# Optimization experiments

Measured on AMD Instinct MI355X. Metric: run time of the kernel, lower is better.

## Reference

```python
import jax, jax.numpy as jnp
from jax import lax
import numpy as np

E = 16          # n_routed_experts
H = 2048        # hidden_size
I = 1408        # moe_intermediate_size
T = 2048        # tokens
K = 6           # top_k


def setup_inputs() -> dict:
    key = jax.random.key(0)
    k1, k2, k3, k4, k5 = jax.random.split(key, 5)
    hidden_states = jax.random.normal(k1, (T, H), dtype=jnp.float32)
    top_k_index = jax.random.randint(k2, (T, K), 0, E)
    top_k_weights = jax.random.uniform(k3, (T, K), dtype=jnp.float32)
    gate_up_proj = jax.random.normal(k4, (E, 2 * I, H), dtype=jnp.float32) * 0.02
    down_proj = jax.random.normal(k5, (E, H, I), dtype=jnp.float32) * 0.02
    return {
        "hidden_states": hidden_states,
        "top_k_index": top_k_index,
        "top_k_weights": top_k_weights,
        "gate_up_proj": gate_up_proj,
        "down_proj": down_proj,
    }


def reference(hidden_states, top_k_index, top_k_weights, gate_up_proj, down_proj):
    # combine[t, e] = sum over k-slots of top_k_weights[t, k] where top_k_index[t, k] == e
    # (scatter-add handles duplicate expert picks identically to index_add_).
    n_tok = hidden_states.shape[0]
    n_exp = gate_up_proj.shape[0]
    combine = jnp.zeros((n_tok, n_exp), hidden_states.dtype)
    combine = combine.at[jnp.arange(n_tok)[:, None], top_k_index].add(top_k_weights)

    def expert_step(acc, params):
        gu, dn, c_e = params  # gu: [2I, H], dn: [H, I], c_e: [n_tok]
        gate, up = jnp.split(hidden_states @ gu.T, 2, axis=-1)  # each [n_tok, I]
        y = (jax.nn.silu(gate) * up) @ dn.T                     # [n_tok, H]
        return acc + y * c_e[:, None], None

    out, _ = lax.scan(
        expert_step,
        jnp.zeros_like(hidden_states),
        (gate_up_proj, down_proj, combine.T),
    )
    return out
```

## Files before the change

kernel.cpp:

```cpp
#include <hip/hip_runtime.h>
#include <hip/hip_bf16.h>
#include <cstdint>

#define T_TOK 2048
#define HD 2048
#define ID 1408
#define NE 16
#define TOPK 6

#define BM 256
#define BK 64
#define BN 32
#define NT1 44
#define NT2 64
#define GMAX 64

typedef __bf16 bf16x8 __attribute__((ext_vector_type(8)));
typedef float f32x4 __attribute__((ext_vector_type(4)));

typedef const __attribute__((address_space(1))) void* gas1_t;
typedef __attribute__((address_space(3))) void* las3_t;
#define GLDS16(g, l) __builtin_amdgcn_global_load_lds((gas1_t)(g), (las3_t)(l), 16, 0, 0)


__global__ void k_combine(const int* __restrict__ idx, const float* __restrict__ w,
                          float* __restrict__ combine) {
    int t = blockIdx.x * blockDim.x + threadIdx.x;
    if (t >= T_TOK) return;
    int ie[TOPK];
    float fw[TOPK];
#pragma unroll
    for (int k = 0; k < TOPK; k++) { ie[k] = idx[t * TOPK + k]; fw[k] = w[t * TOPK + k]; }
#pragma unroll
    for (int e = 0; e < NE; e++) {
        float s = 0.f;
#pragma unroll
        for (int k = 0; k < TOPK; k++) if (ie[k] == e) s += fw[k];
        combine[t * NE + e] = s;
    }
}

__global__ void k_lists(const float* __restrict__ combine, int* __restrict__ counts,
                        int* __restrict__ tok, float* __restrict__ wts) {
    int t = blockIdx.x * blockDim.x + threadIdx.x;
    if (t >= T_TOK) return;
    for (int e = 0; e < NE; e++) {
        float c = combine[t * NE + e];
        if (c != 0.0f) {
            int p = atomicAdd(&counts[e], 1);
            tok[e * T_TOK + p] = t;
            wts[e * T_TOK + p] = c;
        }
    }
}

__global__ void k_cvt(const float* __restrict__ x, __bf16* __restrict__ xb) {
    int i = (blockIdx.x * 256 + threadIdx.x) * 8;
    float4 a = *(const float4*)(x + i);
    float4 b = *(const float4*)(x + i + 4);
    bf16x8 o;
    o[0] = (__bf16)a.x; o[1] = (__bf16)a.y; o[2] = (__bf16)a.z; o[3] = (__bf16)a.w;
    o[4] = (__bf16)b.x; o[5] = (__bf16)b.y; o[6] = (__bf16)b.z; o[7] = (__bf16)b.w;
    *(bf16x8*)(xb + i) = o;
}

__global__ void k_cvtw(const float* __restrict__ src, __bf16* __restrict__ dst, int n8) {
    int stride = gridDim.x * blockDim.x;
    for (int i = blockIdx.x * blockDim.x + threadIdx.x; i < n8; i += stride) {
        size_t o = (size_t)i * 8;
        float4 a = *(const float4*)(src + o);
        float4 b = *(const float4*)(src + o + 4);
        bf16x8 v;
        v[0] = (__bf16)a.x; v[1] = (__bf16)a.y; v[2] = (__bf16)a.z; v[3] = (__bf16)a.w;
        v[4] = (__bf16)b.x; v[5] = (__bf16)b.y; v[6] = (__bf16)b.z; v[7] = (__bf16)b.w;
        *(bf16x8*)(dst + o) = v;
    }
}


__device__ __forceinline__ int swz(int row, int cb) {
    return row * 128 + (cb ^ ((row & 7) << 4));
}

__device__ __forceinline__ bf16x8 ldfrag(const __bf16* base, int row, int cb) {
    return *(const bf16x8*)((const char*)base + swz(row, cb));
}

__device__ __forceinline__ void stage8(const float* __restrict__ src, char* lds,
                                       int row, int cb) {
    float4 f0 = ((const float4*)src)[0];
    float4 f1 = ((const float4*)src)[1];
    bf16x8 o;
    o[0] = (__bf16)f0.x; o[1] = (__bf16)f0.y; o[2] = (__bf16)f0.z; o[3] = (__bf16)f0.w;
    o[4] = (__bf16)f1.x; o[5] = (__bf16)f1.y; o[6] = (__bf16)f1.z; o[7] = (__bf16)f1.w;
    *(bf16x8*)(lds + swz(row, cb)) = o;
}

__device__ __forceinline__ bool decode_item(const int* __restrict__ counts, int it,
                                            int ntn, int& e, int& m, int& n, int& cnt) {
    int r = it;
    for (int ee = 0; ee < NE; ee++) {
        int c = counts[ee];
        int nm = (c + BM - 1) >> 8;
        int tot = nm * ntn;
        if (r < tot) { e = ee; m = r % nm; n = r / nm; cnt = c; return true; }
        r -= tot;
    }
    return false;
}


__global__ __launch_bounds__(256, 4) void k_gemm1_bf16(
    const __bf16* __restrict__ Xb, const __bf16* __restrict__ wgu,
    const int* __restrict__ counts, const int* __restrict__ tok,
    __bf16* __restrict__ act) {
    __shared__ __align__(16) __bf16 sA[BM * BK];
    __shared__ __align__(16) __bf16 sBg[BN * BK];
    __shared__ __align__(16) __bf16 sBu[BN * BK];

    int e, m, n, cnt;
    if (!decode_item(counts, blockIdx.x, NT1, e, m, n, cnt)) return;
    int m0 = m * BM;
    int n0 = n * BN;

    int tid = threadIdx.x;
    int lane = tid & 63;
    int wid = tid >> 6;
    int l15 = lane & 15, lh = lane >> 4;
    int csw = ((lane & 7) ^ ((lane >> 3) & 7)) * 8;

    const __bf16* pA[8];
#pragma unroll
    for (int j = 0; j < 8; j++) {
        int r = 64 * wid + 8 * j + (lane >> 3);
        int g = m0 + r;
        if (g >= cnt) g = cnt - 1;
        pA[j] = Xb + (size_t)tok[e * T_TOK + g] * HD + csw;
    }

    int brow = 8 * wid + (lane >> 3);
    int bsw = ((lane & 7) ^ (lane >> 3)) * 8;
    const __bf16* wbase = wgu + (size_t)e * (2 * ID) * HD;
    const __bf16* pBg = wbase + (size_t)(n0 + brow) * HD + bsw;
    const __bf16* pBu = wbase + (size_t)(ID + n0 + brow) * HD + bsw;

    f32x4 accg[4][2] = {};
    f32x4 accu[4][2] = {};

    for (int k0 = 0; k0 < HD; k0 += BK) {
        __syncthreads();
#pragma unroll
        for (int j = 0; j < 8; j++)
            GLDS16(pA[j] + k0, &sA[(64 * wid + 8 * j) * BK]);
        GLDS16(pBg + k0, &sBg[wid * 512]);
        GLDS16(pBu + k0, &sBu[wid * 512]);
        __syncthreads();
#pragma unroll
        for (int kk = 0; kk < 2; kk++) {
            int cb = kk * 64 + lh * 16;
            bf16x8 a[4];
#pragma unroll
            for (int fm = 0; fm < 4; fm++)
                a[fm] = ldfrag(sA, wid * 64 + fm * 16 + l15, cb);
#pragma unroll
            for (int fn = 0; fn < 2; fn++) {
                bf16x8 bg = ldfrag(sBg, fn * 16 + l15, cb);
                bf16x8 bu = ldfrag(sBu, fn * 16 + l15, cb);
#pragma unroll
                for (int fm = 0; fm < 4; fm++) {
                    accg[fm][fn] = __builtin_amdgcn_mfma_f32_16x16x32_bf16(a[fm], bg, accg[fm][fn], 0, 0, 0);
                    accu[fm][fn] = __builtin_amdgcn_mfma_f32_16x16x32_bf16(a[fm], bu, accu[fm][fn], 0, 0, 0);
                }
            }
        }
    }

#pragma unroll
    for (int fm = 0; fm < 4; fm++) {
#pragma unroll
        for (int fn = 0; fn < 2; fn++) {
#pragma unroll
            for (int j = 0; j < 4; j++) {
                int mloc = wid * 64 + fm * 16 + lh * 4 + j;
                int g = m0 + mloc;
                if (g < cnt) {
                    float gv = accg[fm][fn][j];
                    float uv = accu[fm][fn][j];
                    float sv = gv * (1.0f / (1.0f + __expf(-gv)));
                    int nn = n0 + fn * 16 + l15;
                    act[((size_t)e * T_TOK + g) * ID + nn] = (__bf16)(sv * uv);
                }
            }
        }
    }
}


__global__ __launch_bounds__(256, 4) void k_gemm1_f32(
    const __bf16* __restrict__ Xb, const float* __restrict__ gup,
    const int* __restrict__ counts, const int* __restrict__ tok,
    __bf16* __restrict__ act) {
    __shared__ __align__(16) __bf16 sA[BM * BK];
    __shared__ __align__(16) __bf16 sBg[BN * BK];
    __shared__ __align__(16) __bf16 sBu[BN * BK];

    int e, m, n, cnt;
    if (!decode_item(counts, blockIdx.x, NT1, e, m, n, cnt)) return;
    int m0 = m * BM;
    int n0 = n * BN;

    int tid = threadIdx.x;
    int lane = tid & 63;
    int wid = tid >> 6;
    int l15 = lane & 15, lh = lane >> 4;
    int csw = ((lane & 7) ^ ((lane >> 3) & 7)) * 8;

    const __bf16* pA[8];
#pragma unroll
    for (int j = 0; j < 8; j++) {
        int r = 64 * wid + 8 * j + (lane >> 3);
        int g = m0 + r;
        if (g >= cnt) g = cnt - 1;
        pA[j] = Xb + (size_t)tok[e * T_TOK + g] * HD + csw;
    }

    int br = tid >> 3, bc = tid & 7;
    const float* gbase = gup + (size_t)e * (2 * ID) * HD;
    const float* bgSrc = gbase + (size_t)(n0 + br) * HD + bc * 8;
    const float* buSrc = gbase + (size_t)(ID + n0 + br) * HD + bc * 8;

    f32x4 accg[4][2] = {};
    f32x4 accu[4][2] = {};

    for (int k0 = 0; k0 < HD; k0 += BK) {
        __syncthreads();
#pragma unroll
        for (int j = 0; j < 8; j++)
            GLDS16(pA[j] + k0, &sA[(64 * wid + 8 * j) * BK]);
        stage8(bgSrc + k0, (char*)sBg, br, bc * 16);
        stage8(buSrc + k0, (char*)sBu, br, bc * 16);
        __syncthreads();
#pragma unroll
        for (int kk = 0; kk < 2; kk++) {
            int cb = kk * 64 + lh * 16;
            bf16x8 a[4];
#pragma unroll
            for (int fm = 0; fm < 4; fm++)
                a[fm] = ldfrag(sA, wid * 64 + fm * 16 + l15, cb);
#pragma unroll
            for (int fn = 0; fn < 2; fn++) {
                bf16x8 bg = ldfrag(sBg, fn * 16 + l15, cb);
                bf16x8 bu = ldfrag(sBu, fn * 16 + l15, cb);
#pragma unroll
                for (int fm = 0; fm < 4; fm++) {
                    accg[fm][fn] = __builtin_amdgcn_mfma_f32_16x16x32_bf16(a[fm], bg, accg[fm][fn], 0, 0, 0);
                    accu[fm][fn] = __builtin_amdgcn_mfma_f32_16x16x32_bf16(a[fm], bu, accu[fm][fn], 0, 0, 0);
                }
            }
        }
    }

#pragma unroll
    for (int fm = 0; fm < 4; fm++) {
#pragma unroll
        for (int fn = 0; fn < 2; fn++) {
#pragma unroll
            for (int j = 0; j < 4; j++) {
                int mloc = wid * 64 + fm * 16 + lh * 4 + j;
                int g = m0 + mloc;
                if (g < cnt) {
                    float gv = accg[fm][fn][j];
                    float uv = accu[fm][fn][j];
                    float sv = gv * (1.0f / (1.0f + __expf(-gv)));
                    int nn = n0 + fn * 16 + l15;
                    act[((size_t)e * T_TOK + g) * ID + nn] = (__bf16)(sv * uv);
                }
            }
        }
    }
}


__global__ __launch_bounds__(256, 4) void k_gemm2_bf16(
    const __bf16* __restrict__ act, const __bf16* __restrict__ wdn,
    const int* __restrict__ counts, const int* __restrict__ tok,
    const float* __restrict__ wts, float* __restrict__ out) {
    __shared__ __align__(16) __bf16 sA[BM * BK];
    __shared__ __align__(16) __bf16 sB[BN * BK];
    __shared__ int tokLds[BM];
    __shared__ float wtLds[BM];

    int e, m, n, cnt;
    if (!decode_item(counts, blockIdx.x, NT2, e, m, n, cnt)) return;
    int m0 = m * BM;
    int n0 = n * BN;

    int tid = threadIdx.x;
    int lane = tid & 63;
    int wid = tid >> 6;
    int l15 = lane & 15, lh = lane >> 4;
    int csw = ((lane & 7) ^ ((lane >> 3) & 7)) * 8;

    if (tid < BM) {
        int g = m0 + tid;
        bool v = g < cnt;
        tokLds[tid] = v ? tok[e * T_TOK + g] : 0;
        wtLds[tid] = v ? wts[e * T_TOK + g] : 0.f;
    }

    const __bf16* pA[8];
#pragma unroll
    for (int j = 0; j < 8; j++) {
        int r = 64 * wid + 8 * j + (lane >> 3);
        int g = m0 + r;
        if (g >= cnt) g = cnt - 1;
        pA[j] = act + ((size_t)e * T_TOK + g) * ID + csw;
    }

    int brow = 8 * wid + (lane >> 3);
    int bsw = ((lane & 7) ^ (lane >> 3)) * 8;
    const __bf16* pB = wdn + ((size_t)e * HD + (n0 + brow)) * ID + bsw;

    f32x4 acc[4][2] = {};

    for (int k0 = 0; k0 < ID; k0 += BK) {
        __syncthreads();
#pragma unroll
        for (int j = 0; j < 8; j++)
            GLDS16(pA[j] + k0, &sA[(64 * wid + 8 * j) * BK]);
        GLDS16(pB + k0, &sB[wid * 512]);
        __syncthreads();
#pragma unroll
        for (int kk = 0; kk < 2; kk++) {
            int cb = kk * 64 + lh * 16;
            bf16x8 a[4];
#pragma unroll
            for (int fm = 0; fm < 4; fm++)
                a[fm] = ldfrag(sA, wid * 64 + fm * 16 + l15, cb);
#pragma unroll
            for (int fn = 0; fn < 2; fn++) {
                bf16x8 b = ldfrag(sB, fn * 16 + l15, cb);
#pragma unroll
                for (int fm = 0; fm < 4; fm++)
                    acc[fm][fn] = __builtin_amdgcn_mfma_f32_16x16x32_bf16(a[fm], b, acc[fm][fn], 0, 0, 0);
            }
        }
    }

    __syncthreads();
#pragma unroll
    for (int fm = 0; fm < 4; fm++) {
#pragma unroll
        for (int fn = 0; fn < 2; fn++) {
#pragma unroll
            for (int j = 0; j < 4; j++) {
                int mloc = wid * 64 + fm * 16 + lh * 4 + j;
                int g = m0 + mloc;
                if (g < cnt) {
                    float v = acc[fm][fn][j] * wtLds[mloc];
                    int nn = n0 + fn * 16 + l15;
                    atomicAdd(&out[(size_t)tokLds[mloc] * HD + nn], v);
                }
            }
        }
    }
}


__global__ __launch_bounds__(256, 4) void k_gemm2_f32(
    const __bf16* __restrict__ act, const float* __restrict__ dn,
    const int* __restrict__ counts, const int* __restrict__ tok,
    const float* __restrict__ wts, float* __restrict__ out) {
    __shared__ __align__(16) __bf16 sA[BM * BK];
    __shared__ __align__(16) __bf16 sB[BN * BK];
    __shared__ int tokLds[BM];
    __shared__ float wtLds[BM];

    int e, m, n, cnt;
    if (!decode_item(counts, blockIdx.x, NT2, e, m, n, cnt)) return;
    int m0 = m * BM;
    int n0 = n * BN;

    int tid = threadIdx.x;
    int lane = tid & 63;
    int wid = tid >> 6;
    int l15 = lane & 15, lh = lane >> 4;
    int csw = ((lane & 7) ^ ((lane >> 3) & 7)) * 8;

    if (tid < BM) {
        int g = m0 + tid;
        bool v = g < cnt;
        tokLds[tid] = v ? tok[e * T_TOK + g] : 0;
        wtLds[tid] = v ? wts[e * T_TOK + g] : 0.f;
    }

    const __bf16* pA[8];
#pragma unroll
    for (int j = 0; j < 8; j++) {
        int r = 64 * wid + 8 * j + (lane >> 3);
        int g = m0 + r;
        if (g >= cnt) g = cnt - 1;
        pA[j] = act + ((size_t)e * T_TOK + g) * ID + csw;
    }

    int br = tid >> 3, bc = tid & 7;
    const float* bSrc = dn + (size_t)e * HD * ID + (size_t)(n0 + br) * ID + bc * 8;

    f32x4 acc[4][2] = {};

    for (int k0 = 0; k0 < ID; k0 += BK) {
        __syncthreads();
#pragma unroll
        for (int j = 0; j < 8; j++)
            GLDS16(pA[j] + k0, &sA[(64 * wid + 8 * j) * BK]);
        stage8(bSrc + k0, (char*)sB, br, bc * 16);
        __syncthreads();
#pragma unroll
        for (int kk = 0; kk < 2; kk++) {
            int cb = kk * 64 + lh * 16;
            bf16x8 a[4];
#pragma unroll
            for (int fm = 0; fm < 4; fm++)
                a[fm] = ldfrag(sA, wid * 64 + fm * 16 + l15, cb);
#pragma unroll
            for (int fn = 0; fn < 2; fn++) {
                bf16x8 b = ldfrag(sB, fn * 16 + l15, cb);
#pragma unroll
                for (int fm = 0; fm < 4; fm++)
                    acc[fm][fn] = __builtin_amdgcn_mfma_f32_16x16x32_bf16(a[fm], b, acc[fm][fn], 0, 0, 0);
            }
        }
    }

    __syncthreads();
#pragma unroll
    for (int fm = 0; fm < 4; fm++) {
#pragma unroll
        for (int fn = 0; fn < 2; fn++) {
#pragma unroll
            for (int j = 0; j < 4; j++) {
                int mloc = wid * 64 + fm * 16 + lh * 4 + j;
                int g = m0 + mloc;
                if (g < cnt) {
                    float v = acc[fm][fn][j] * wtLds[mloc];
                    int nn = n0 + fn * 16 + l15;
                    atomicAdd(&out[(size_t)tokLds[mloc] * HD + nn], v);
                }
            }
        }
    }
}


extern "C" void kernel_launch(void* const* d_in, const int* in_sizes, int n_in,
                              void* d_out, int out_size, void* d_ws, size_t ws_size,
                              hipStream_t stream) {
    const float* hs = (const float*)d_in[0];
    const int* tki = (const int*)d_in[1];
    const float* tkw = (const float*)d_in[2];
    const float* gup = (const float*)d_in[3];
    const float* dnp = (const float*)d_in[4];
    float* out = (float*)d_out;

    const size_t nGU = (size_t)NE * (2 * ID) * HD;
    const size_t nDN = (size_t)NE * HD * ID;

    char* p = (char*)d_ws;
    int* counts = (int*)p;      p += 256;
    float* combine = (float*)p; p += (size_t)T_TOK * NE * 4;
    int* tok = (int*)p;         p += (size_t)NE * T_TOK * 4;
    float* wts = (float*)p;     p += (size_t)NE * T_TOK * 4;
    __bf16* Xb = (__bf16*)p;    p += (size_t)T_TOK * HD * 2;
    __bf16* act = (__bf16*)p;   p += (size_t)NE * T_TOK * ID * 2;
    size_t used_base = (size_t)(p - (char*)d_ws);
    __bf16* wgu = (__bf16*)p;
    __bf16* wdn = (__bf16*)(p + nGU * 2);

    bool cvt_gu = ws_size >= used_base + nGU * 2;
    bool cvt_dn = ws_size >= used_base + nGU * 2 + nDN * 2;

    hipMemsetAsync(counts, 0, 256, stream);
    hipMemsetAsync(d_out, 0, (size_t)T_TOK * HD * 4, stream);
    k_combine<<<T_TOK / 256, 256, 0, stream>>>(tki, tkw, combine);
    k_lists<<<T_TOK / 256, 256, 0, stream>>>(combine, counts, tok, wts);
    k_cvt<<<(T_TOK * HD / 8) / 256, 256, 0, stream>>>(hs, Xb);

    if (cvt_gu) {
        k_cvtw<<<2048, 256, 0, stream>>>(gup, wgu, (int)(nGU / 8));
        k_gemm1_bf16<<<dim3(GMAX * NT1), 256, 0, stream>>>(Xb, wgu, counts, tok, act);
    } else {
        k_gemm1_f32<<<dim3(GMAX * NT1), 256, 0, stream>>>(Xb, gup, counts, tok, act);
    }

    if (cvt_dn) {
        k_cvtw<<<2048, 256, 0, stream>>>(dnp, wdn, (int)(nDN / 8));
        k_gemm2_bf16<<<dim3(GMAX * NT2), 256, 0, stream>>>(act, wdn, counts, tok, wts, out);
    } else {
        k_gemm2_f32<<<dim3(GMAX * NT2), 256, 0, stream>>>(act, dnp, counts, tok, wts, out);
    }
}
```

Measured before the change: 507.8 us.

## Double-buffer LDS in bf16 MoE GEMMs and widen gemm2 N tile

```diff
diff --git a/kernel.cpp b/kernel.cpp
--- a/kernel.cpp
+++ b/kernel.cpp
@@ -10,9 +10,11 @@
 
 #define BM 256
 #define BK 64
-#define BN 32
+#define BN1 32
+#define BN2 64
 #define NT1 44
-#define NT2 64
+#define NT2 32
+#define NT2F 64
 #define GMAX 64
 
 typedef __bf16 bf16x8 __attribute__((ext_vector_type(8)));
@@ -110,18 +112,18 @@
 }
 
 
-__global__ __launch_bounds__(256, 4) void k_gemm1_bf16(
+__global__ __launch_bounds__(256, 2) void k_gemm1_bf16(
     const __bf16* __restrict__ Xb, const __bf16* __restrict__ wgu,
     const int* __restrict__ counts, const int* __restrict__ tok,
     __bf16* __restrict__ act) {
-    __shared__ __align__(16) __bf16 sA[BM * BK];
-    __shared__ __align__(16) __bf16 sBg[BN * BK];
-    __shared__ __align__(16) __bf16 sBu[BN * BK];
+    __shared__ __align__(16) __bf16 sA[2][BM * BK];
+    __shared__ __align__(16) __bf16 sBg[2][BN1 * BK];
+    __shared__ __align__(16) __bf16 sBu[2][BN1 * BK];
 
     int e, m, n, cnt;
     if (!decode_item(counts, blockIdx.x, NT1, e, m, n, cnt)) return;
     int m0 = m * BM;
-    int n0 = n * BN;
+    int n0 = n * BN1;
 
     int tid = threadIdx.x;
     int lane = tid & 63;
@@ -147,25 +149,39 @@
     f32x4 accg[4][2] = {};
     f32x4 accu[4][2] = {};
 
-    for (int k0 = 0; k0 < HD; k0 += BK) {
-        __syncthreads();
-#pragma unroll
-        for (int j = 0; j < 8; j++)
-            GLDS16(pA[j] + k0, &sA[(64 * wid + 8 * j) * BK]);
-        GLDS16(pBg + k0, &sBg[wid * 512]);
-        GLDS16(pBu + k0, &sBu[wid * 512]);
-        __syncthreads();
+    const int NT = HD / BK;
+
+#pragma unroll
+    for (int j = 0; j < 8; j++)
+        GLDS16(pA[j], &sA[0][(64 * wid + 8 * j) * BK]);
+    GLDS16(pBg, &sBg[0][wid * 512]);
+    GLDS16(pBu, &sBu[0][wid * 512]);
+    __syncthreads();
+
+    for (int k = 0; k < NT; k++) {
+        int cur = k & 1, nxt = cur ^ 1;
+        if (k + 1 < NT) {
+            int k0 = (k + 1) * BK;
+#pragma unroll
+            for (int j = 0; j < 8; j++)
+                GLDS16(pA[j] + k0, &sA[nxt][(64 * wid + 8 * j) * BK]);
+            GLDS16(pBg + k0, &sBg[nxt][wid * 512]);
+            GLDS16(pBu + k0, &sBu[nxt][wid * 512]);
+        }
+        const __bf16* sAc = sA[cur];
+        const __bf16* sBgc = sBg[cur];
+        const __bf16* sBuc = sBu[cur];
 #pragma unroll
         for (int kk = 0; kk < 2; kk++) {
             int cb = kk * 64 + lh * 16;
             bf16x8 a[4];
 #pragma unroll
             for (int fm = 0; fm < 4; fm++)
-                a[fm] = ldfrag(sA, wid * 64 + fm * 16 + l15, cb);
+                a[fm] = ldfrag(sAc, wid * 64 + fm * 16 + l15, cb);
 #pragma unroll
             for (int fn = 0; fn < 2; fn++) {
-                bf16x8 bg = ldfrag(sBg, fn * 16 + l15, cb);
-                bf16x8 bu = ldfrag(sBu, fn * 16 + l15, cb);
+                bf16x8 bg = ldfrag(sBgc, fn * 16 + l15, cb);
+                bf16x8 bu = ldfrag(sBuc, fn * 16 + l15, cb);
 #pragma unroll
                 for (int fm = 0; fm < 4; fm++) {
                     accg[fm][fn] = __builtin_amdgcn_mfma_f32_16x16x32_bf16(a[fm], bg, accg[fm][fn], 0, 0, 0);
@@ -173,6 +189,7 @@
                 }
             }
         }
+        __syncthreads();
     }
 
 #pragma unroll
@@ -196,18 +213,116 @@
 }
 
 
+__global__ __launch_bounds__(256, 2) void k_gemm2_bf16(
+    const __bf16* __restrict__ act, const __bf16* __restrict__ wdn,
+    const int* __restrict__ counts, const int* __restrict__ tok,
+    const float* __restrict__ wts, float* __restrict__ out) {
+    __shared__ __align__(16) __bf16 sA[2][BM * BK];
+    __shared__ __align__(16) __bf16 sB[2][BN2 * BK];
+
+    int e, m, n, cnt;
+    if (!decode_item(counts, blockIdx.x, NT2, e, m, n, cnt)) return;
+    int m0 = m * BM;
+    int n0 = n * BN2;
+
+    int tid = threadIdx.x;
+    int lane = tid & 63;
+    int wid = tid >> 6;
+    int l15 = lane & 15, lh = lane >> 4;
+    int csw = ((lane & 7) ^ ((lane >> 3) & 7)) * 8;
+
+    const __bf16* pA[8];
+#pragma unroll
+    for (int j = 0; j < 8; j++) {
+        int r = 64 * wid + 8 * j + (lane >> 3);
+        int g = m0 + r;
+        if (g >= cnt) g = cnt - 1;
+        pA[j] = act + ((size_t)e * T_TOK + g) * ID + csw;
+    }
+
+    int bsw = ((lane & 7) ^ (lane >> 3)) * 8;
+    const __bf16* pB[2];
+#pragma unroll
+    for (int c = 0; c < 2; c++) {
+        int r = 16 * wid + 8 * c + (lane >> 3);
+        pB[c] = wdn + ((size_t)e * HD + (n0 + r)) * ID + bsw;
+    }
+
+    f32x4 acc[4][4] = {};
+
+    const int NT = ID / BK;
+
+#pragma unroll
+    for (int j = 0; j < 8; j++)
+        GLDS16(pA[j], &sA[0][(64 * wid + 8 * j) * BK]);
+#pragma unroll
+    for (int c = 0; c < 2; c++)
+        GLDS16(pB[c], &sB[0][(16 * wid + 8 * c) * BK]);
+    __syncthreads();
+
+    for (int k = 0; k < NT; k++) {
+        int cur = k & 1, nxt = cur ^ 1;
+        if (k + 1 < NT) {
+            int k0 = (k + 1) * BK;
+#pragma unroll
+            for (int j = 0; j < 8; j++)
+                GLDS16(pA[j] + k0, &sA[nxt][(64 * wid + 8 * j) * BK]);
+#pragma unroll
+            for (int c = 0; c < 2; c++)
+                GLDS16(pB[c] + k0, &sB[nxt][(16 * wid + 8 * c) * BK]);
+        }
+        const __bf16* sAc = sA[cur];
+        const __bf16* sBc = sB[cur];
+#pragma unroll
+        for (int kk = 0; kk < 2; kk++) {
+            int cb = kk * 64 + lh * 16;
+            bf16x8 a[4];
+#pragma unroll
+            for (int fm = 0; fm < 4; fm++)
+                a[fm] = ldfrag(sAc, wid * 64 + fm * 16 + l15, cb);
+#pragma unroll
+            for (int fn = 0; fn < 4; fn++) {
+                bf16x8 b = ldfrag(sBc, fn * 16 + l15, cb);
+#pragma unroll
+                for (int fm = 0; fm < 4; fm++)
+                    acc[fm][fn] = __builtin_amdgcn_mfma_f32_16x16x32_bf16(a[fm], b, acc[fm][fn], 0, 0, 0);
+            }
+        }
+        __syncthreads();
+    }
+
+#pragma unroll
+    for (int fm = 0; fm < 4; fm++) {
+#pragma unroll
+        for (int j = 0; j < 4; j++) {
+            int mloc = wid * 64 + fm * 16 + lh * 4 + j;
+            int g = m0 + mloc;
+            if (g < cnt) {
+                int t = tok[e * T_TOK + g];
+                float w = wts[e * T_TOK + g];
+#pragma unroll
+                for (int fn = 0; fn < 4; fn++) {
+                    int nn = n0 + fn * 16 + l15;
+                    atomicAdd(&out[(size_t)t * HD + nn], acc[fm][fn][j] * w);
+                }
+            }
+        }
+    }
+}
+
+
 __global__ __launch_bounds__(256, 4) void k_gemm1_f32(
     const __bf16* __restrict__ Xb, const float* __restrict__ gup,
     const int* __restrict__ counts, const int* __restrict__ tok,
     __bf16* __restrict__ act) {
     __shared__ __align__(16) __bf16 sA[BM * BK];
-    __shared__ __align__(16) __bf16 sBg[BN * BK];
-    __shared__ __align__(16) __bf16 sBu[BN * BK];
+    __shared__ __align__(16) __bf16 sBg[BN1 * BK];
+    __shared__ __align__(16) __bf16 sBu[BN1 * BK];
 
     int e, m, n, cnt;
     if (!decode_item(counts, blockIdx.x, NT1, e, m, n, cnt)) return;
     int m0 = m * BM;
-    int n0 = n * BN;
+    int n0 = n * BN1;
 
     int tid = threadIdx.x;
     int lane = tid & 63;
@@ -280,20 +395,17 @@
     }
 }
 
-
-__global__ __launch_bounds__(256, 4) void k_gemm2_bf16(
-    const __bf16* __restrict__ act, const __bf16* __restrict__ wdn,
+__global__ __launch_bounds__(256, 4) void k_gemm2_f32(
+    const __bf16* __restrict__ act, const float* __restrict__ dn,
     const int* __restrict__ counts, const int* __restrict__ tok,
     const float* __restrict__ wts, float* __restrict__ out) {
     __shared__ __align__(16) __bf16 sA[BM * BK];
-    __shared__ __align__(16) __bf16 sB[BN * BK];
-    __shared__ int tokLds[BM];
-    __shared__ float wtLds[BM];
+    __shared__ __align__(16) __bf16 sB[32 * BK];
 
     int e, m, n, cnt;
-    if (!decode_item(counts, blockIdx.x, NT2, e, m, n, cnt)) return;
+    if (!decode_item(counts, blockIdx.x, NT2F, e, m, n, cnt)) return;
     int m0 = m * BM;
-    int n0 = n * BN;
+    int n0 = n * 32;
 
     int tid = threadIdx.x;
     int lane = tid & 63;
@@ -301,13 +413,6 @@
     int l15 = lane & 15, lh = lane >> 4;
     int csw = ((lane & 7) ^ ((lane >> 3) & 7)) * 8;
 
-    if (tid < BM) {
-        int g = m0 + tid;
-        bool v = g < cnt;
-        tokLds[tid] = v ? tok[e * T_TOK + g] : 0;
-        wtLds[tid] = v ? wts[e * T_TOK + g] : 0.f;
-    }
-
     const __bf16* pA[8];
 #pragma unroll
     for (int j = 0; j < 8; j++) {
@@ -317,92 +422,6 @@
         pA[j] = act + ((size_t)e * T_TOK + g) * ID + csw;
     }
 
-    int brow = 8 * wid + (lane >> 3);
-    int bsw = ((lane & 7) ^ (lane >> 3)) * 8;
-    const __bf16* pB = wdn + ((size_t)e * HD + (n0 + brow)) * ID + bsw;
-
-    f32x4 acc[4][2] = {};
-
-    for (int k0 = 0; k0 < ID; k0 += BK) {
-        __syncthreads();
-#pragma unroll
-        for (int j = 0; j < 8; j++)
-            GLDS16(pA[j] + k0, &sA[(64 * wid + 8 * j) * BK]);
-        GLDS16(pB + k0, &sB[wid * 512]);
-        __syncthreads();
-#pragma unroll
-        for (int kk = 0; kk < 2; kk++) {
-            int cb = kk * 64 + lh * 16;
-            bf16x8 a[4];
-#pragma unroll
-            for (int fm = 0; fm < 4; fm++)
-                a[fm] = ldfrag(sA, wid * 64 + fm * 16 + l15, cb);
-#pragma unroll
-            for (int fn = 0; fn < 2; fn++) {
-                bf16x8 b = ldfrag(sB, fn * 16 + l15, cb);
-#pragma unroll
-                for (int fm = 0; fm < 4; fm++)
-                    acc[fm][fn] = __builtin_amdgcn_mfma_f32_16x16x32_bf16(a[fm], b, acc[fm][fn], 0, 0, 0);
-            }
-        }
-    }
-
-    __syncthreads();
-#pragma unroll
-    for (int fm = 0; fm < 4; fm++) {
-#pragma unroll
-        for (int fn = 0; fn < 2; fn++) {
-#pragma unroll
-            for (int j = 0; j < 4; j++) {
-                int mloc = wid * 64 + fm * 16 + lh * 4 + j;
-                int g = m0 + mloc;
-                if (g < cnt) {
-                    float v = acc[fm][fn][j] * wtLds[mloc];
-                    int nn = n0 + fn * 16 + l15;
-                    atomicAdd(&out[(size_t)tokLds[mloc] * HD + nn], v);
-                }
-            }
-        }
-    }
-}
-
-
-__global__ __launch_bounds__(256, 4) void k_gemm2_f32(
-    const __bf16* __restrict__ act, const float* __restrict__ dn,
-    const int* __restrict__ counts, const int* __restrict__ tok,
-    const float* __restrict__ wts, float* __restrict__ out) {
-    __shared__ __align__(16) __bf16 sA[BM * BK];
-    __shared__ __align__(16) __bf16 sB[BN * BK];
-    __shared__ int tokLds[BM];
-    __shared__ float wtLds[BM];
-
-    int e, m, n, cnt;
-    if (!decode_item(counts, blockIdx.x, NT2, e, m, n, cnt)) return;
-    int m0 = m * BM;
-    int n0 = n * BN;
-
-    int tid = threadIdx.x;
-    int lane = tid & 63;
-    int wid = tid >> 6;
-    int l15 = lane & 15, lh = lane >> 4;
-    int csw = ((lane & 7) ^ ((lane >> 3) & 7)) * 8;
-
-    if (tid < BM) {
-        int g = m0 + tid;
-        bool v = g < cnt;
-        tokLds[tid] = v ? tok[e * T_TOK + g] : 0;
-        wtLds[tid] = v ? wts[e * T_TOK + g] : 0.f;
-    }
-
-    const __bf16* pA[8];
-#pragma unroll
-    for (int j = 0; j < 8; j++) {
-        int r = 64 * wid + 8 * j + (lane >> 3);
-        int g = m0 + r;
-        if (g >= cnt) g = cnt - 1;
-        pA[j] = act + ((size_t)e * T_TOK + g) * ID + csw;
-    }
-
     int br = tid >> 3, bc = tid & 7;
     const float* bSrc = dn + (size_t)e * HD * ID + (size_t)(n0 + br) * ID + bc * 8;
 
@@ -436,15 +455,16 @@
 #pragma unroll
     for (int fm = 0; fm < 4; fm++) {
 #pragma unroll
-        for (int fn = 0; fn < 2; fn++) {
-#pragma unroll
-            for (int j = 0; j < 4; j++) {
-                int mloc = wid * 64 + fm * 16 + lh * 4 + j;
-                int g = m0 + mloc;
-                if (g < cnt) {
-                    float v = acc[fm][fn][j] * wtLds[mloc];
+        for (int j = 0; j < 4; j++) {
+            int mloc = wid * 64 + fm * 16 + lh * 4 + j;
+            int g = m0 + mloc;
+            if (g < cnt) {
+                int t = tok[e * T_TOK + g];
+                float w = wts[e * T_TOK + g];
+#pragma unroll
+                for (int fn = 0; fn < 2; fn++) {
                     int nn = n0 + fn * 16 + l15;
-                    atomicAdd(&out[(size_t)tokLds[mloc] * HD + nn], v);
+                    atomicAdd(&out[(size_t)t * HD + nn], acc[fm][fn][j] * w);
                 }
             }
         }
@@ -496,6 +516,6 @@
         k_cvtw<<<2048, 256, 0, stream>>>(dnp, wdn, (int)(nDN / 8));
         k_gemm2_bf16<<<dim3(GMAX * NT2), 256, 0, stream>>>(act, wdn, counts, tok, wts, out);
     } else {
-        k_gemm2_f32<<<dim3(GMAX * NT2), 256, 0, stream>>>(act, dnp, counts, tok, wts, out);
-    }
-}
+        k_gemm2_f32<<<dim3(GMAX * NT2F), 256, 0, stream>>>(act, dnp, counts, tok, wts, out);
+    }
+}
```

Result: slower. 630.1 us (+24.1%).
